# Kernel tuning notes

Measured on AMD Instinct MI355X. Metric: run time of the kernel, lower is better.

Reference implementation:

```python
import jax, jax.numpy as jnp
import numpy as np

B, T, C = 4, 2048, 1024
H = 16
HD = C // H  # 64


def setup_inputs() -> dict:
    key = jax.random.key(0)
    k1, k2, k3 = jax.random.split(key, 3)
    x = jax.random.normal(k1, (B, T, C), dtype=jnp.float32)
    # learned params (torch Linear y = x @ W.T stored here as [in, out])
    Wqkv = jax.random.normal(k2, (C, 3 * C), dtype=jnp.float32) * (C ** -0.5)
    Wout = jax.random.normal(k3, (C, C), dtype=jnp.float32) * (C ** -0.5)
    bout = jnp.zeros((C,), dtype=jnp.float32)
    causal_mask = jnp.tril(jnp.ones((1, 1, T, T), dtype=bool))
    return {"x": x, "causal_mask": causal_mask, "Wqkv": Wqkv, "Wout": Wout, "bout": bout}


def reference(x, causal_mask, Wqkv, Wout, bout):
    b, t, c = x.shape
    scale = HD ** -0.5
    qkv = x @ Wqkv  # [B,T,3C]
    q, k, v = jnp.split(qkv, 3, axis=-1)
    # [B,T,C] -> [B,H,T,hd]
    q = q.reshape(b, t, H, HD).transpose(0, 2, 1, 3)
    k = k.reshape(b, t, H, HD).transpose(0, 2, 1, 3)
    v = v.reshape(b, t, H, HD).transpose(0, 2, 1, 3)
    att = jnp.einsum("bhqd,bhkd->bhqk", q, k) * scale  # [B,H,T,T]
    att = jnp.where(causal_mask, att, -jnp.inf)
    att = jax.nn.softmax(att, axis=-1)
    # dropout in eval mode == identity
    out = jnp.einsum("bhqk,bhkd->bhqd", att, v)  # [B,H,T,hd]
    out = out.transpose(0, 2, 1, 3).reshape(b, t, c)
    return out @ Wout + bout


if __name__ == "__main__":
    inp = setup_inputs()
    y = jax.jit(reference)(**inp)
    print(y.shape, y.dtype)
```

## Files before the change

kernel.cpp:

```cpp
#include <hip/hip_runtime.h>
#include <hip/hip_bf16.h>
#include <stdint.h>


typedef __bf16 bf16;
typedef __bf16 bf16x4 __attribute__((ext_vector_type(4)));
typedef __bf16 bf16x8 __attribute__((ext_vector_type(8)));
typedef float floatx4 __attribute__((ext_vector_type(4)));
typedef float floatx16 __attribute__((ext_vector_type(16)));
typedef unsigned int uintx4 __attribute__((ext_vector_type(4)));

#define MFMA16(a, b, c) __builtin_amdgcn_mfma_f32_16x16x32_bf16(a, b, c, 0, 0, 0)
#define MFMA32(a, b, c) __builtin_amdgcn_mfma_f32_32x32x16_bf16(a, b, c, 0, 0, 0)

#if defined(__has_builtin)
#if __has_builtin(__builtin_amdgcn_global_load_lds)
#define HAS_GLL 1
#endif
#endif

#ifdef HAS_GLL
__device__ __forceinline__ void gll16(const bf16* g, bf16* l) {
  __builtin_amdgcn_global_load_lds(
      (const __attribute__((address_space(1))) unsigned int*)g,
      (__attribute__((address_space(3))) unsigned int*)l, 16, 0, 0);
}
#endif

__device__ __forceinline__ unsigned cvtpk(float lo, float hi) {
  unsigned r;
  asm("v_cvt_pk_bf16_f32 %0, %1, %2" : "=v"(r) : "v"(lo), "v"(hi));
  return r;
}
__device__ __forceinline__ void pl32swap(unsigned& a, unsigned& b) {
  asm volatile("v_permlane32_swap_b32 %0, %1" : "+v"(a), "+v"(b));
}

__global__ __launch_bounds__(256)
void convert_x(const float* __restrict__ in, bf16* __restrict__ out) {
  const size_t i = (size_t)blockIdx.x * 256 + threadIdx.x;
  const float4* p = (const float4*)in + i * 2;
  float4 a = p[0], b = p[1];
  bf16x8 v;
  v[0] = (bf16)a.x; v[1] = (bf16)a.y; v[2] = (bf16)a.z; v[3] = (bf16)a.w;
  v[4] = (bf16)b.x; v[5] = (bf16)b.y; v[6] = (bf16)b.z; v[7] = (bf16)b.w;
  *((bf16x8*)out + i) = v;
}

__global__ __launch_bounds__(256)
void transpose_w(const float* __restrict__ W, bf16* __restrict__ Wt, int K, int N) {
  __shared__ bf16 tile[32][33];
  const int k0 = blockIdx.y * 32, n0 = blockIdx.x * 32;
  const int t = threadIdx.x;
  {
    const int r = t >> 3, c4 = (t & 7) * 4;
    float4 v = *(const float4*)(W + (size_t)(k0 + r) * N + n0 + c4);
    tile[r][c4 + 0] = (bf16)v.x;
    tile[r][c4 + 1] = (bf16)v.y;
    tile[r][c4 + 2] = (bf16)v.z;
    tile[r][c4 + 3] = (bf16)v.w;
  }
  __syncthreads();
  {
    const int nr = t >> 3, kc = (t & 7) * 4;
    bf16x4 o;
#pragma unroll
    for (int j = 0; j < 4; ++j) o[j] = tile[kc + j][nr];
    *(bf16x4*)(Wt + (size_t)(n0 + nr) * K + k0 + kc) = o;
  }
}

template <int MODE>
__global__ __launch_bounds__(256, 3)
void gemm_bt(const bf16* __restrict__ A, const bf16* __restrict__ Bt,
             const float* __restrict__ bias, void* __restrict__ Cv,
             bf16* __restrict__ Vout, int M, int N, int K) {
  __shared__ __align__(16) bf16 As[128 * 64];
  __shared__ __align__(16) bf16 Bs[128 * 64];

  const int t = threadIdx.x, lane = t & 63, w = t >> 6;
  const int m_ = lane & 15, quad = lane >> 4;
  const int wm = w >> 1, wn = w & 1;
  const int m0 = blockIdx.y * 128, n0 = blockIdx.x * 128;

  floatx4 acc[4][4];
#pragma unroll
  for (int i = 0; i < 4; ++i)
#pragma unroll
    for (int j = 0; j < 4; ++j) {
      floatx4 z = {0.f, 0.f, 0.f, 0.f};
      acc[i][j] = z;
    }

  for (int k0 = 0; k0 < K; k0 += 64) {
#pragma unroll
    for (int i = 0; i < 4; ++i) {
      const int R0 = i * 32 + w * 8;
      const int R = R0 + (lane >> 3);
      const int sg = (lane & 7) ^ (R & 7);
      const bf16* ga = A + (size_t)(m0 + R) * K + k0 + sg * 8;
      const bf16* gb = Bt + (size_t)(n0 + R) * K + k0 + sg * 8;
#ifdef HAS_GLL
      gll16(ga, As + (size_t)R0 * 64);
      gll16(gb, Bs + (size_t)R0 * 64);
#else
      *(bf16x8*)(As + (size_t)R * 64 + (lane & 7) * 8) = *(const bf16x8*)ga;
      *(bf16x8*)(Bs + (size_t)R * 64 + (lane & 7) * 8) = *(const bf16x8*)gb;
#endif
    }
    __syncthreads();

#pragma unroll
    for (int kc = 0; kc < 2; ++kc) {
      bf16x8 af[4], bfr[4];
#pragma unroll
      for (int mt = 0; mt < 4; ++mt) {
        const int r = wm * 64 + mt * 16 + m_;
        const int slot = ((kc << 2) | quad) ^ (r & 7);
        af[mt] = *(const bf16x8*)(As + (size_t)r * 64 + slot * 8);
      }
#pragma unroll
      for (int nt = 0; nt < 4; ++nt) {
        const int rn = wn * 64 + nt * 16 + m_;
        const int slot = ((kc << 2) | quad) ^ (rn & 7);
        bfr[nt] = *(const bf16x8*)(Bs + (size_t)rn * 64 + slot * 8);
      }
#pragma unroll
      for (int mt = 0; mt < 4; ++mt)
#pragma unroll
        for (int nt = 0; nt < 4; ++nt)
          acc[mt][nt] = MFMA16(af[mt], bfr[nt], acc[mt][nt]);
    }
    __syncthreads();
  }

  if (MODE == 0) {
#pragma unroll
    for (int mt = 0; mt < 4; ++mt)
#pragma unroll
      for (int nt = 0; nt < 4; ++nt) {
        const int col = n0 + wn * 64 + nt * 16 + m_;
        const float bv = bias[col];
#pragma unroll
        for (int r = 0; r < 4; ++r) {
          const int row = m0 + wm * 64 + mt * 16 + quad * 4 + r;
          ((float*)Cv)[(size_t)row * N + col] = acc[mt][nt][r] + bv;
        }
      }
  } else {
    if (n0 < 2048) {
      const float sc = (n0 < 1024) ? 0.18033688f : 1.0f;
#pragma unroll
      for (int mt = 0; mt < 4; ++mt)
#pragma unroll
        for (int nt = 0; nt < 4; ++nt) {
          const int col = n0 + wn * 64 + nt * 16 + m_;
#pragma unroll
          for (int r = 0; r < 4; ++r) {
            const int row = m0 + wm * 64 + mt * 16 + quad * 4 + r;
            ((bf16*)Cv)[(size_t)row * 2048 + col] = (bf16)(acc[mt][nt][r] * sc);
          }
        }
    } else {
#pragma unroll
      for (int mt = 0; mt < 4; ++mt) {
        const int rowb = m0 + wm * 64 + mt * 16 + quad * 4;
        const int bb = rowb >> 11, tok = rowb & 2047;
#pragma unroll
        for (int nt = 0; nt < 4; ++nt) {
          const int c = n0 - 2048 + wn * 64 + nt * 16 + m_;
          const int h = c >> 6, d = c & 63;
          bf16x4 pw;
#pragma unroll
          for (int r = 0; r < 4; ++r) pw[r] = (bf16)acc[mt][nt][r];
          *(bf16x4*)(Vout + ((size_t)(bb * 16 + h) * 64 + d) * 2048 + tok) = pw;
        }
      }
    }
  }
}

__device__ __forceinline__ void stage64(const bf16* base, bf16* lds,
                                        int lane, int w) {
#pragma unroll
  for (int i = 0; i < 2; ++i) {
    const int seg = w * 2 + i;
    const int row = seg * 8 + (lane >> 3);
    const int g = (lane & 7) ^ (row & 7);
#ifdef HAS_GLL
    gll16(base + (size_t)row * 2048 + g * 8, lds + seg * 512);
#else
    *(bf16x8*)(lds + row * 64 + (lane & 7) * 8) =
        *(const bf16x8*)(base + (size_t)row * 2048 + g * 8);
#endif
  }
}

__global__ __launch_bounds__(256, 2)
void attn_fwd(const bf16* __restrict__ qk, const bf16* __restrict__ vtp,
              bf16* __restrict__ attnout) {
  __shared__ __align__(16) bf16 KsB[2][64 * 64];
  __shared__ __align__(16) bf16 VTB[2][64 * 64];

  const int t = threadIdx.x, lane = t & 63, w = t >> 6;
  const int ln = lane & 31, hi = lane >> 5;
  const int bh = blockIdx.x;
  const int qbmap[16] = {15, 14, 13, 12, 8, 9, 10, 11, 7, 6, 5, 4, 0, 1, 2, 3};
  const int qb = qbmap[blockIdx.y];
  const int b = bh >> 4, h = bh & 15;

  const bf16* Qp = qk + (size_t)b * 2048 * 2048 + h * 64;
  const bf16* Kp = qk + (size_t)b * 2048 * 2048 + 1024 + h * 64;
  const bf16* Vt = vtp + (size_t)bh * 64 * 2048;

  const int q0w = qb * 128 + w * 32;

  bf16x8 qf[4];
#pragma unroll
  for (int st = 0; st < 4; ++st)
    qf[st] = *(const bf16x8*)(Qp + (size_t)(q0w + ln) * 2048 + st * 16 + hi * 8);

  bf16x8 ones;
#pragma unroll
  for (int j = 0; j < 8; ++j) ones[j] = (bf16)1.0f;

  floatx16 o[2];
#pragma unroll
  for (int nt = 0; nt < 2; ++nt)
#pragma unroll
    for (int r = 0; r < 16; ++r) o[nt][r] = 0.f;
  floatx16 lacc;
#pragma unroll
  for (int r = 0; r < 16; ++r) lacc[r] = 0.f;

  const int nch = 2 * qb + 2;

  stage64(Kp, KsB[0], lane, w);
  stage64(Vt, VTB[0], lane, w);

  for (int ch = 0; ch < nch; ++ch) {
    const int kb = ch * 64;
    const int cur = ch & 1;
    __syncthreads();
    if (ch + 1 < nch) {
      stage64(Kp + (size_t)(kb + 64) * 2048, KsB[cur ^ 1], lane, w);
      stage64(Vt + kb + 64, VTB[cur ^ 1], lane, w);
    }
    if (kb > q0w + 31) continue;
    const bf16* Kb = KsB[cur];
    const bf16* Vb = VTB[cur];
    const bool need_mask = (kb + 63 > q0w);

#pragma unroll
    for (int kt = 0; kt < 2; ++kt) {
      if (kb + kt * 32 <= q0w + 31) {
        floatx16 s;
#pragma unroll
        for (int r = 0; r < 16; ++r) s[r] = 0.f;
        const int krow = kt * 32 + ln;
        __builtin_amdgcn_s_setprio(1);
#pragma unroll
        for (int st = 0; st < 4; ++st) {
          const bf16x8 kf = *(const bf16x8*)(
              Kb + krow * 64 + ((((st << 1) | hi) ^ (krow & 7)) << 3));
          s = MFMA32(kf, qf[st], s);
        }
        __builtin_amdgcn_s_setprio(0);
        if (need_mask) {
          const int qg = q0w + ln;
          const int kbase = kb + kt * 32 + 4 * hi;
#pragma unroll
          for (int rq = 0; rq < 4; ++rq)
#pragma unroll
            for (int j = 0; j < 4; ++j)
              if (kbase + 8 * rq + j > qg) s[rq * 4 + j] = -1e30f;
        }
#pragma unroll
        for (int sb = 0; sb < 2; ++sb) {
          unsigned A0 = cvtpk(exp2f(s[8 * sb + 0]), exp2f(s[8 * sb + 1]));
          unsigned A1 = cvtpk(exp2f(s[8 * sb + 2]), exp2f(s[8 * sb + 3]));
          unsigned B0 = cvtpk(exp2f(s[8 * sb + 4]), exp2f(s[8 * sb + 5]));
          unsigned B1 = cvtpk(exp2f(s[8 * sb + 6]), exp2f(s[8 * sb + 7]));
          pl32swap(A0, B0);
          pl32swap(A1, B1);
          uintx4 fw;
          fw[0] = A0; fw[1] = A1; fw[2] = B0; fw[3] = B1;
          const bf16x8 paf = __builtin_bit_cast(bf16x8, fw);
          const int st = kt * 2 + sb;
          __builtin_amdgcn_s_setprio(1);
          lacc = MFMA32(paf, ones, lacc);
#pragma unroll
          for (int nt = 0; nt < 2; ++nt) {
            const int vrow = nt * 32 + ln;
            const bf16x8 vf = *(const bf16x8*)(
                Vb + vrow * 64 + ((((st << 1) | hi) ^ (vrow & 7)) << 3));
            o[nt] = MFMA32(paf, vf, o[nt]);
          }
          __builtin_amdgcn_s_setprio(0);
        }
      }
    }
  }

  floatx16 linv;
#pragma unroll
  for (int r = 0; r < 16; ++r) linv[r] = 1.0f / lacc[r];

#pragma unroll
  for (int nt = 0; nt < 2; ++nt) {
#pragma unroll
    for (int rq = 0; rq < 4; ++rq) {
#pragma unroll
      for (int j = 0; j < 4; ++j) {
        const int row = q0w + 8 * rq + 4 * hi + j;
        attnout[((size_t)b * 2048 + row) * 1024 + h * 64 + nt * 32 + ln] =
            (bf16)(o[nt][rq * 4 + j] * linv[rq * 4 + j]);
      }
    }
  }
}

extern "C" void kernel_launch(void* const* d_in, const int* in_sizes, int n_in,
                              void* d_out, int out_size, void* d_ws, size_t ws_size,
                              hipStream_t stream) {
  (void)in_sizes; (void)n_in; (void)out_size; (void)ws_size;
  const float* x    = (const float*)d_in[0];
  const float* Wqkv = (const float*)d_in[2];
  const float* Wout = (const float*)d_in[3];
  const float* bout = (const float*)d_in[4];
  float* out = (float*)d_out;

  bf16* qk      = (bf16*)d_ws;
  bf16* vtp     = (bf16*)((char*)d_ws + (size_t)32 * 1024 * 1024);
  bf16* attnout = (bf16*)((char*)d_ws + (size_t)48 * 1024 * 1024);
  bf16* Wout_t  = (bf16*)d_ws;
  bf16* xbf    = (bf16*)d_out;
  bf16* Wqkv_t = (bf16*)d_out + (size_t)8192 * 1024;

  convert_x<<<4096, 256, 0, stream>>>(x, xbf);
  transpose_w<<<dim3(96, 32), 256, 0, stream>>>(Wqkv, Wqkv_t, 1024, 3072);

  gemm_bt<1><<<dim3(24, 64), 256, 0, stream>>>(xbf, Wqkv_t, nullptr, qk, vtp,
                                               8192, 3072, 1024);
  attn_fwd<<<dim3(64, 16), 256, 0, stream>>>(qk, vtp, attnout);

  transpose_w<<<dim3(32, 32), 256, 0, stream>>>(Wout, Wout_t, 1024, 1024);
  gemm_bt<0><<<dim3(8, 64), 256, 0, stream>>>(attnout, Wout_t, bout, out,
                                              nullptr, 8192, 1024, 1024);
}
```

Before: 243.5 us.

## Load K and V fragments directly from global memory instead of LDS staging

Removes the double-buffered LDS staging of K and V tiles and the per-chunk block barrier. Each wave now reads its K and V MFMA fragments straight from global memory and iterates only over the key chunks its own query rows need. This removes barrier stalls and the work imbalance between waves, but each of the four waves in a block now fetches the same K/V data separately, relying on L1/L2 to absorb the repeated reads. The global loads also lose the prefetch overlap the staged pipeline provided.

After: 320.9 us. 31.8% more time.

```diff
diff --git a/kernel.cpp b/kernel.cpp
--- a/kernel.cpp
+++ b/kernel.cpp
@@ -180,40 +180,21 @@
   }
 }
 
-__device__ __forceinline__ void stage64(const bf16* base, bf16* lds,
-                                        int lane, int w) {
-#pragma unroll
-  for (int i = 0; i < 2; ++i) {
-    const int seg = w * 2 + i;
-    const int row = seg * 8 + (lane >> 3);
-    const int g = (lane & 7) ^ (row & 7);
-#ifdef HAS_GLL
-    gll16(base + (size_t)row * 2048 + g * 8, lds + seg * 512);
-#else
-    *(bf16x8*)(lds + row * 64 + (lane & 7) * 8) =
-        *(const bf16x8*)(base + (size_t)row * 2048 + g * 8);
-#endif
-  }
-}
-
 __global__ __launch_bounds__(256, 2)
 void attn_fwd(const bf16* __restrict__ qk, const bf16* __restrict__ vtp,
               bf16* __restrict__ attnout) {
-  __shared__ __align__(16) bf16 KsB[2][64 * 64];
-  __shared__ __align__(16) bf16 VTB[2][64 * 64];
-
   const int t = threadIdx.x, lane = t & 63, w = t >> 6;
   const int ln = lane & 31, hi = lane >> 5;
   const int bh = blockIdx.x;
   const int qbmap[16] = {15, 14, 13, 12, 8, 9, 10, 11, 7, 6, 5, 4, 0, 1, 2, 3};
-  const int qb = qbmap[blockIdx.y];
+  const int qt = qbmap[blockIdx.y] * 4 + w;
   const int b = bh >> 4, h = bh & 15;
 
   const bf16* Qp = qk + (size_t)b * 2048 * 2048 + h * 64;
   const bf16* Kp = qk + (size_t)b * 2048 * 2048 + 1024 + h * 64;
   const bf16* Vt = vtp + (size_t)bh * 64 * 2048;
 
-  const int q0w = qb * 128 + w * 32;
+  const int q0w = qt * 32;
 
   bf16x8 qf[4];
 #pragma unroll
@@ -233,38 +214,27 @@
 #pragma unroll
   for (int r = 0; r < 16; ++r) lacc[r] = 0.f;
 
-  const int nch = 2 * qb + 2;
-
-  stage64(Kp, KsB[0], lane, w);
-  stage64(Vt, VTB[0], lane, w);
+  const int nch = (q0w >> 6) + 1;
 
   for (int ch = 0; ch < nch; ++ch) {
     const int kb = ch * 64;
-    const int cur = ch & 1;
-    __syncthreads();
-    if (ch + 1 < nch) {
-      stage64(Kp + (size_t)(kb + 64) * 2048, KsB[cur ^ 1], lane, w);
-      stage64(Vt + kb + 64, VTB[cur ^ 1], lane, w);
-    }
-    if (kb > q0w + 31) continue;
-    const bf16* Kb = KsB[cur];
-    const bf16* Vb = VTB[cur];
     const bool need_mask = (kb + 63 > q0w);
 
 #pragma unroll
     for (int kt = 0; kt < 2; ++kt) {
       if (kb + kt * 32 <= q0w + 31) {
+        const int krow = kb + kt * 32 + ln;
+        const bf16* kp = Kp + (size_t)krow * 2048 + hi * 8;
+        bf16x8 kf[4];
+#pragma unroll
+        for (int st = 0; st < 4; ++st)
+          kf[st] = *(const bf16x8*)(kp + st * 16);
         floatx16 s;
 #pragma unroll
         for (int r = 0; r < 16; ++r) s[r] = 0.f;
-        const int krow = kt * 32 + ln;
         __builtin_amdgcn_s_setprio(1);
 #pragma unroll
-        for (int st = 0; st < 4; ++st) {
-          const bf16x8 kf = *(const bf16x8*)(
-              Kb + krow * 64 + ((((st << 1) | hi) ^ (krow & 7)) << 3));
-          s = MFMA32(kf, qf[st], s);
-        }
+        for (int st = 0; st < 4; ++st) s = MFMA32(kf[st], qf[st], s);
         __builtin_amdgcn_s_setprio(0);
         if (need_mask) {
           const int qg = q0w + ln;
@@ -286,14 +256,14 @@
           uintx4 fw;
           fw[0] = A0; fw[1] = A1; fw[2] = B0; fw[3] = B1;
           const bf16x8 paf = __builtin_bit_cast(bf16x8, fw);
-          const int st = kt * 2 + sb;
+          const int stt = kt * 2 + sb;
+          const bf16* vp = Vt + kb + stt * 16 + hi * 8;
           __builtin_amdgcn_s_setprio(1);
           lacc = MFMA32(paf, ones, lacc);
 #pragma unroll
           for (int nt = 0; nt < 2; ++nt) {
-            const int vrow = nt * 32 + ln;
-            const bf16x8 vf = *(const bf16x8*)(
-                Vb + vrow * 64 + ((((st << 1) | hi) ^ (vrow & 7)) << 3));
+            const bf16x8 vf =
+                *(const bf16x8*)(vp + (size_t)(nt * 32 + ln) * 2048);
             o[nt] = MFMA32(paf, vf, o[nt]);
           }
           __builtin_amdgcn_s_setprio(0);
```

## Merge x conversion and Wqkv transpose into one launch; vectorize out-proj stores

Applied to the files above, without the earlier changes.

Replaces the convert_x and transpose_w(Wqkv) launches with a single prologue kernel whose block index selects either the x-to-bf16 conversion or a 32x32 weight-tile transpose, saving one kernel launch and the gap between the two. Separately, the output-projection GEMM swaps the MFMA operands so each lane holds four consecutive columns of one row. This allows float4 bias loads and float4 output stores in place of scalar strided writes. The prologue now declares shared memory for every block, including the conversion blocks that never use it.

New measurement: 257.5 us. 1.06x slower.

```diff
diff --git a/kernel.cpp b/kernel.cpp
--- a/kernel.cpp
+++ b/kernel.cpp
@@ -37,14 +37,39 @@
 }
 
 __global__ __launch_bounds__(256)
-void convert_x(const float* __restrict__ in, bf16* __restrict__ out) {
-  const size_t i = (size_t)blockIdx.x * 256 + threadIdx.x;
-  const float4* p = (const float4*)in + i * 2;
-  float4 a = p[0], b = p[1];
-  bf16x8 v;
-  v[0] = (bf16)a.x; v[1] = (bf16)a.y; v[2] = (bf16)a.z; v[3] = (bf16)a.w;
-  v[4] = (bf16)b.x; v[5] = (bf16)b.y; v[6] = (bf16)b.z; v[7] = (bf16)b.w;
-  *((bf16x8*)out + i) = v;
+void prologue(const float* __restrict__ x, bf16* __restrict__ xbf,
+              const float* __restrict__ Wqkv, bf16* __restrict__ Wqkv_t) {
+  __shared__ bf16 tile[32][33];
+  const int t = threadIdx.x;
+  if (blockIdx.x < 4096) {
+    const size_t i = (size_t)blockIdx.x * 256 + t;
+    const float4* p = (const float4*)x + i * 2;
+    float4 a = p[0], b = p[1];
+    bf16x8 v;
+    v[0] = (bf16)a.x; v[1] = (bf16)a.y; v[2] = (bf16)a.z; v[3] = (bf16)a.w;
+    v[4] = (bf16)b.x; v[5] = (bf16)b.y; v[6] = (bf16)b.z; v[7] = (bf16)b.w;
+    *((bf16x8*)xbf + i) = v;
+  } else {
+    const int tb = blockIdx.x - 4096;
+    const int n0 = (tb % 96) * 32;
+    const int k0 = (tb / 96) * 32;
+    {
+      const int r = t >> 3, c4 = (t & 7) * 4;
+      float4 v = *(const float4*)(Wqkv + (size_t)(k0 + r) * 3072 + n0 + c4);
+      tile[r][c4 + 0] = (bf16)v.x;
+      tile[r][c4 + 1] = (bf16)v.y;
+      tile[r][c4 + 2] = (bf16)v.z;
+      tile[r][c4 + 3] = (bf16)v.w;
+    }
+    __syncthreads();
+    {
+      const int nr = t >> 3, kc = (t & 7) * 4;
+      bf16x4 o;
+#pragma unroll
+      for (int j = 0; j < 4; ++j) o[j] = tile[kc + j][nr];
+      *(bf16x4*)(Wqkv_t + (size_t)(n0 + nr) * 1024 + k0 + kc) = o;
+    }
+  }
 }
 
 __global__ __launch_bounds__(256)
@@ -128,25 +153,32 @@
 #pragma unroll
       for (int mt = 0; mt < 4; ++mt)
 #pragma unroll
-        for (int nt = 0; nt < 4; ++nt)
-          acc[mt][nt] = MFMA16(af[mt], bfr[nt], acc[mt][nt]);
+        for (int nt = 0; nt < 4; ++nt) {
+          if (MODE == 0)
+            acc[mt][nt] = MFMA16(bfr[nt], af[mt], acc[mt][nt]);
+          else
+            acc[mt][nt] = MFMA16(af[mt], bfr[nt], acc[mt][nt]);
+        }
     }
     __syncthreads();
   }
 
   if (MODE == 0) {
 #pragma unroll
-    for (int mt = 0; mt < 4; ++mt)
+    for (int mt = 0; mt < 4; ++mt) {
+      const int row = m0 + wm * 64 + mt * 16 + m_;
 #pragma unroll
       for (int nt = 0; nt < 4; ++nt) {
-        const int col = n0 + wn * 64 + nt * 16 + m_;
-        const float bv = bias[col];
-#pragma unroll
-        for (int r = 0; r < 4; ++r) {
-          const int row = m0 + wm * 64 + mt * 16 + quad * 4 + r;
-          ((float*)Cv)[(size_t)row * N + col] = acc[mt][nt][r] + bv;
-        }
-      }
+        const int colb = n0 + wn * 64 + nt * 16 + quad * 4;
+        const float4 bv = *(const float4*)(bias + colb);
+        float4 ov;
+        ov.x = acc[mt][nt][0] + bv.x;
+        ov.y = acc[mt][nt][1] + bv.y;
+        ov.z = acc[mt][nt][2] + bv.z;
+        ov.w = acc[mt][nt][3] + bv.w;
+        *(float4*)((float*)Cv + (size_t)row * N + colb) = ov;
+      }
+    }
   } else {
     if (n0 < 2048) {
       const float sc = (n0 < 1024) ? 0.18033688f : 1.0f;
@@ -337,8 +369,7 @@
   bf16* xbf    = (bf16*)d_out;
   bf16* Wqkv_t = (bf16*)d_out + (size_t)8192 * 1024;
 
-  convert_x<<<4096, 256, 0, stream>>>(x, xbf);
-  transpose_w<<<dim3(96, 32), 256, 0, stream>>>(Wqkv, Wqkv_t, 1024, 3072);
+  prologue<<<7168, 256, 0, stream>>>(x, xbf, Wqkv, Wqkv_t);
 
   gemm_bt<1><<<dim3(24, 64), 256, 0, stream>>>(xbf, Wqkv_t, nullptr, qk, vtp,
                                                8192, 3072, 1024);
```
